# Kernel optimization log

Measured on AMD Instinct MI355X. Metric: run time of the kernel, lower is better.

The kernel has to match this reference:

```python
import jax, jax.numpy as jnp
import numpy as np

B = 8          # batch
RES = 64       # resolution (H = W)
DIM = 512      # channels
HEADS = 8
HD = DIM // HEADS   # 64
HSP, WSP = RES, 8   # idx=0: H_sp=resolution, W_sp=split_size
NH, NW = RES // HSP, RES // WSP   # windows per axis


def setup_inputs() -> dict:
    key = jax.random.key(0)
    k1, k2, k3 = jax.random.split(key, 3)
    qkv = jax.random.normal(k1, (3, B, RES * RES, DIM), dtype=jnp.float32)
    lepe_w = jax.random.normal(k2, (DIM, 1, 3, 3), dtype=jnp.float32) * 0.1
    lepe_b = jax.random.normal(k3, (DIM,), dtype=jnp.float32) * 0.1
    return {"qkv": qkv, "lepe_w": lepe_w, "lepe_b": lepe_b}


def _to_windows(t):
    # [B, L, C] row-major -> [B*NH*NW, HSP*WSP, C]; equivalent to the
    # block-diagonal flex_attention mask grouping (y//H_sp, x//W_sp).
    t = t.reshape(B, NH, HSP, NW, WSP, DIM)
    return t.transpose(0, 1, 3, 2, 4, 5).reshape(B * NH * NW, HSP * WSP, DIM)


def _from_windows(t):
    t = t.reshape(B, NH, NW, HSP, WSP, DIM).transpose(0, 1, 3, 2, 4, 5)
    return t.reshape(B, RES * RES, DIM)


def reference(qkv, lepe_w, lepe_b):
    q, k, v = qkv[0], qkv[1], qkv[2]            # each [B, L, C]
    qw, kw, vw = _to_windows(q), _to_windows(k), _to_windows(v)

    # LePE: depthwise 3x3 conv on v laid out per-window as [n, C, HSP, WSP]
    vimg = vw.transpose(0, 2, 1).reshape(-1, DIM, HSP, WSP)
    lepe = jax.lax.conv_general_dilated(
        vimg, lepe_w, window_strides=(1, 1), padding='SAME',
        dimension_numbers=('NCHW', 'OIHW', 'NCHW'), feature_group_count=DIM)
    lepe = lepe + lepe_b[None, :, None, None]
    lepe = lepe.reshape(-1, DIM, HSP * WSP).transpose(0, 2, 1)  # [n, T, C]

    def split_heads(t):
        return t.reshape(t.shape[0], t.shape[1], HEADS, HD)

    qh, kh, vh, lh = map(split_heads, (qw, kw, vw, lepe))
    scale = 1.0 / np.sqrt(HD).astype(np.float32)  # flex_attention default scale
    scores = jnp.einsum('wqhd,wkhd->whqk', qh, kh) * scale
    attn = jax.nn.softmax(scores, axis=-1)
    out = jnp.einsum('whqk,wkhd->wqhd', attn, vh) + lh   # [n, T, H, hd]
    out = out.reshape(out.shape[0], out.shape[1], DIM)
    return _from_windows(out)
```

## Files before the change

kernel.cpp:

```cpp
#include <hip/hip_runtime.h>
#include <hip/hip_bf16.h>

#define DIMV 512
#define HDV  64
#define VSTR 524
#define VT_BASE 65536
#define SMEM_B (VT_BASE + 64 * VSTR * 2)

typedef __bf16 bf16x8_t __attribute__((ext_vector_type(8)));
typedef float f32x4_t __attribute__((ext_vector_type(4)));

union Frag { bf16x8_t v; unsigned short u[8]; unsigned int w[4]; uint2 d[2]; uint4 q; };

static __device__ __forceinline__ unsigned short f2bf(float f) {
  return __builtin_bit_cast(unsigned short, (__bf16)f);
}
static __device__ __forceinline__ float bf2f(unsigned int h) {
  return __builtin_bit_cast(float, h << 16);
}

#define BARRIER_NODRAIN() asm volatile("s_waitcnt lgkmcnt(0)\n\ts_barrier" ::: "memory")

__global__ __launch_bounds__(1024, 4)
void lepe_attn_kernel(const float* __restrict__ qkv,
                      const float* __restrict__ lw,
                      const float* __restrict__ lb,
                      float* __restrict__ out)
{
  __shared__ __align__(16) unsigned char smem[SMEM_B];

  const int head = blockIdx.x >> 6;
  const int win  = blockIdx.x & 63;
  const int bat  = win >> 3;
  const int nw   = win & 7;

  const int tid  = threadIdx.x;
  const int wave = tid >> 6, lane = tid & 63;
  const int l15  = lane & 15, g = lane >> 4;

  const float* qptr = qkv;
  const float* kptr = qkv + 16777216;
  const float* vptr = qkv + 33554432;
  const int rowbase = bat * 4096;

  auto grow = [&](int tok) -> int {
    return rowbase + ((tok >> 3) << 6) + (nw << 3) + (tok & 7);
  };

  const int s_t = tid >> 4;
  const int s_c = (tid & 15) * 4;
  const size_t GSTRIDE = 262144;
  const float* kg = kptr + (size_t)grow(s_t) * DIMV + head * HDV + s_c;
  const float* vg = vptr + (size_t)grow(s_t) * DIMV + head * HDV + s_c;
  const int kwbase = s_t * 128 + ((s_c * 2) ^ ((s_t & 7) << 4));

  float4 ck0, ck1, cv0, cv1;
  auto issueC = [&](int c) {
    ck0 = *(const float4*)(kg + (size_t)(2 * c) * GSTRIDE);
    ck1 = *(const float4*)(kg + (size_t)(2 * c + 1) * GSTRIDE);
    cv0 = *(const float4*)(vg + (size_t)(2 * c) * GSTRIDE);
    cv1 = *(const float4*)(vg + (size_t)(2 * c + 1) * GSTRIDE);
  };
  auto writeC = [&](int c) {
    uint2 kp;
    kp.x = (unsigned)f2bf(ck0.x) | ((unsigned)f2bf(ck0.y) << 16);
    kp.y = (unsigned)f2bf(ck0.z) | ((unsigned)f2bf(ck0.w) << 16);
    *(uint2*)(smem + (2 * c) * 8192 + kwbase) = kp;
    kp.x = (unsigned)f2bf(ck1.x) | ((unsigned)f2bf(ck1.y) << 16);
    kp.y = (unsigned)f2bf(ck1.z) | ((unsigned)f2bf(ck1.w) << 16);
    *(uint2*)(smem + (2 * c + 1) * 8192 + kwbase) = kp;
    unsigned short* vt = (unsigned short*)(smem + VT_BASE);
    #pragma unroll
    for (int gi = 0; gi < 2; ++gi) {
      const float4 vv = gi ? cv1 : cv0;
      const int t = (2 * c + gi) * 64 + s_t;
      float fv[4] = {vv.x, vv.y, vv.z, vv.w};
      #pragma unroll
      for (int i = 0; i < 4; ++i)
        vt[(s_c + i) * VSTR + t] = f2bf(fv[i]);
    }
  };

  issueC(0);

  const float QSC = 0.1803368801f;
  const int qbase = wave * 32;
  float4 qin[8];
  #pragma unroll
  for (int qi = 0; qi < 2; ++qi) {
    const float* qp = qptr + (size_t)grow(qbase + qi * 16 + l15) * DIMV + head * HDV;
    #pragma unroll
    for (int kc = 0; kc < 2; ++kc) {
      qin[qi * 4 + kc * 2 + 0] = *(const float4*)(qp + kc * 32 + 8 * g);
      qin[qi * 4 + kc * 2 + 1] = *(const float4*)(qp + kc * 32 + 8 * g + 4);
    }
  }

  writeC(0);

  Frag qf[2][2];
  #pragma unroll
  for (int qi = 0; qi < 2; ++qi)
    #pragma unroll
    for (int kc = 0; kc < 2; ++kc) {
      const float4 f0 = qin[qi * 4 + kc * 2 + 0];
      const float4 f1 = qin[qi * 4 + kc * 2 + 1];
      qf[qi][kc].u[0] = f2bf(f0.x * QSC); qf[qi][kc].u[1] = f2bf(f0.y * QSC);
      qf[qi][kc].u[2] = f2bf(f0.z * QSC); qf[qi][kc].u[3] = f2bf(f0.w * QSC);
      qf[qi][kc].u[4] = f2bf(f1.x * QSC); qf[qi][kc].u[5] = f2bf(f1.y * QSC);
      qf[qi][kc].u[6] = f2bf(f1.z * QSC); qf[qi][kc].u[7] = f2bf(f1.w * QSC);
    }

  __syncthreads();

  const f32x4_t zero4 = {0.f, 0.f, 0.f, 0.f};
  f32x4_t ot[4][2];
  #pragma unroll
  for (int di = 0; di < 4; ++di)
    #pragma unroll
    for (int qi = 0; qi < 2; ++qi) ot[di][qi] = zero4;
  float lsumA[2] = {0.f, 0.f};
  float lsumB[2] = {0.f, 0.f};

  const int ksw = (l15 & 7) << 4;

  #pragma unroll
  for (int c = 0; c < 4; ++c) {
    if (c < 3) issueC(c + 1);

    #pragma unroll
    for (int t4 = 0; t4 < 4; ++t4) {
      const int kt = c * 4 + t4;

      Frag kf[2][2];
      #pragma unroll
      for (int ki = 0; ki < 2; ++ki) {
        const unsigned char* rowp = smem + (kt * 32 + ki * 16 + l15) * 128;
        #pragma unroll
        for (int kc = 0; kc < 2; ++kc)
          kf[ki][kc].q = *(const uint4*)(rowp + ((kc * 64 + g * 16) ^ ksw));
      }

      f32x4_t st[2][2];
      #pragma unroll
      for (int ki = 0; ki < 2; ++ki)
        #pragma unroll
        for (int qi = 0; qi < 2; ++qi) st[ki][qi] = zero4;

      #pragma unroll
      for (int kc = 0; kc < 2; ++kc)
        #pragma unroll
        for (int ki = 0; ki < 2; ++ki)
          #pragma unroll
          for (int qi = 0; qi < 2; ++qi)
            st[ki][qi] = __builtin_amdgcn_mfma_f32_16x16x32_bf16(
                kf[ki][kc].v, qf[qi][kc].v, st[ki][qi], 0, 0, 0);

      #pragma unroll
      for (int ki = 0; ki < 2; ++ki)
        #pragma unroll
        for (int qi = 0; qi < 2; ++qi) {
          f32x4_t s = st[ki][qi];
          #pragma unroll
          for (int r = 0; r < 4; ++r) {
            float pr = __builtin_amdgcn_exp2f(s[r]);
            s[r] = pr;
            if (ki == 0) lsumA[qi] += pr;
            else         lsumB[qi] += pr;
          }
          st[ki][qi] = s;
        }

      Frag vf[4];
      #pragma unroll
      for (int di = 0; di < 4; ++di) {
        const unsigned char* vp = smem + VT_BASE + (di * 16 + l15) * (VSTR * 2)
                                  + kt * 64 + 8 * g;
        vf[di].d[0] = *(const uint2*)(vp);
        vf[di].d[1] = *(const uint2*)(vp + 32);
      }

      #pragma unroll
      for (int qi = 0; qi < 2; ++qi) {
        Frag pb;
        #pragma unroll
        for (int r = 0; r < 4; ++r) {
          pb.u[r]     = f2bf(st[0][qi][r]);
          pb.u[4 + r] = f2bf(st[1][qi][r]);
        }
        #pragma unroll
        for (int di = 0; di < 4; ++di)
          ot[di][qi] = __builtin_amdgcn_mfma_f32_16x16x32_bf16(
              vf[di].v, pb.v, ot[di][qi], 0, 0, 0);
      }
    }

    if (c < 3) { writeC(c + 1); BARRIER_NODRAIN(); }
  }

  float rl[2];
  #pragma unroll
  for (int qi = 0; qi < 2; ++qi) {
    float s = lsumA[qi] + lsumB[qi];
    s += __shfl_xor(s, 16, 64);
    s += __shfl_xor(s, 32, 64);
    rl[qi] = 1.0f / s;
  }

  float lout[32];
  {
    float wgt[9];
    const float* wp = lw + (size_t)(head * HDV + lane) * 9;
    #pragma unroll
    for (int i = 0; i < 9; ++i) wgt[i] = wp[i];
    const float bias = lb[head * HDV + lane];
    const int yb = wave * 4;
    const unsigned char* vrow = smem + VT_BASE + lane * (VSTR * 2);

    float rm[8], rc[8], rp2[8];
    auto loadrow = [&](int y, float* dst) {
      if ((unsigned)y < 64u) {
        const unsigned char* pp = vrow + y * 16;
        unsigned a0 = *(const unsigned*)(pp);
        unsigned a1 = *(const unsigned*)(pp + 4);
        unsigned a2 = *(const unsigned*)(pp + 8);
        unsigned a3 = *(const unsigned*)(pp + 12);
        dst[0] = bf2f(a0 & 0xffffu); dst[1] = bf2f(a0 >> 16);
        dst[2] = bf2f(a1 & 0xffffu); dst[3] = bf2f(a1 >> 16);
        dst[4] = bf2f(a2 & 0xffffu); dst[5] = bf2f(a2 >> 16);
        dst[6] = bf2f(a3 & 0xffffu); dst[7] = bf2f(a3 >> 16);
      } else {
        #pragma unroll
        for (int x = 0; x < 8; ++x) dst[x] = 0.f;
      }
    };
    loadrow(yb - 1, rm);
    loadrow(yb, rc);
    #pragma unroll
    for (int yy = 0; yy < 4; ++yy) {
      loadrow(yb + yy + 1, rp2);
      #pragma unroll
      for (int x = 0; x < 8; ++x) {
        float acc = bias;
        if (x > 0) acc += rm[x-1]*wgt[0] + rc[x-1]*wgt[3] + rp2[x-1]*wgt[6];
        acc += rm[x]*wgt[1] + rc[x]*wgt[4] + rp2[x]*wgt[7];
        if (x < 7) acc += rm[x+1]*wgt[2] + rc[x+1]*wgt[5] + rp2[x+1]*wgt[8];
        lout[yy * 8 + x] = acc;
      }
      #pragma unroll
      for (int x = 0; x < 8; ++x) { rm[x] = rc[x]; rc[x] = rp2[x]; }
    }
  }

  BARRIER_NODRAIN();

  unsigned char* bp = smem + wave * 4352;
  #pragma unroll
  for (int t = 0; t < 32; ++t)
    *(unsigned short*)(bp + t * 136 + 2 * lane) = f2bf(lout[t]);
  BARRIER_NODRAIN();

  #pragma unroll
  for (int qi = 0; qi < 2; ++qi) {
    const float rlq = rl[qi];
    const int tl = qi * 16 + l15;
    float* op = out + (size_t)grow(qbase + tl) * DIMV + head * HDV;
    #pragma unroll
    for (int di = 0; di < 4; ++di) {
      uint2 lv = *(const uint2*)(bp + tl * 136 + di * 32 + 8 * g);
      float4 o;
      o.x = ot[di][qi][0] * rlq + bf2f(lv.x & 0xffffu);
      o.y = ot[di][qi][1] * rlq + bf2f(lv.x >> 16);
      o.z = ot[di][qi][2] * rlq + bf2f(lv.y & 0xffffu);
      o.w = ot[di][qi][3] * rlq + bf2f(lv.y >> 16);
      *(float4*)(op + di * 16 + 4 * g) = o;
    }
  }
}

extern "C" void kernel_launch(void* const* d_in, const int* in_sizes, int n_in,
                              void* d_out, int out_size, void* d_ws, size_t ws_size,
                              hipStream_t stream) {
  const float* qkv = (const float*)d_in[0];
  const float* lw  = (const float*)d_in[1];
  const float* lb  = (const float*)d_in[2];
  float* out = (float*)d_out;
  (void)in_sizes; (void)n_in; (void)out_size; (void)d_ws; (void)ws_size;

  dim3 grid(512);
  dim3 block(1024);
  hipLaunchKernelGGL(lepe_attn_kernel, grid, block, 0, stream, qkv, lw, lb, out);
}
```

Baseline: 76.36 us.

## Store K and V in fragment-native swizzled LDS tiles for single 128-bit reads

Reorganizes the shared-memory layout of K and transposed V into per-tile, MFMA-fragment-ordered blocks with XOR swizzles, so each lane reads its K and V operand fragments with one 128-bit LDS load each instead of several smaller strided loads. The store side now computes fragment-ordered addresses, and the LePE convolution row loader is rewritten to read from the new V layout. The aim is fewer LDS instructions and fewer bank conflicts in the inner attention loop. In exchange the scattered 16-bit V stores become more complex, and LDS use changes slightly (128 KB total).

```diff
diff --git a/kernel.cpp b/kernel.cpp
--- a/kernel.cpp
+++ b/kernel.cpp
@@ -3,9 +3,8 @@
 
 #define DIMV 512
 #define HDV  64
-#define VSTR 524
-#define VT_BASE 65536
-#define SMEM_B (VT_BASE + 64 * VSTR * 2)
+#define VBASE 65536
+#define SMEM_B 131072
 
 typedef __bf16 bf16x8_t __attribute__((ext_vector_type(8)));
 typedef float f32x4_t __attribute__((ext_vector_type(4)));
@@ -17,6 +16,12 @@
 }
 static __device__ __forceinline__ float bf2f(unsigned int h) {
   return __builtin_bit_cast(float, h << 16);
+}
+static __device__ __forceinline__ uint2 pack4(const float4 f) {
+  uint2 r;
+  r.x = (unsigned)f2bf(f.x) | ((unsigned)f2bf(f.y) << 16);
+  r.y = (unsigned)f2bf(f.z) | ((unsigned)f2bf(f.w) << 16);
+  return r;
 }
 
 #define BARRIER_NODRAIN() asm volatile("s_waitcnt lgkmcnt(0)\n\ts_barrier" ::: "memory")
@@ -52,7 +57,20 @@
   const size_t GSTRIDE = 262144;
   const float* kg = kptr + (size_t)grow(s_t) * DIMV + head * HDV + s_c;
   const float* vg = vptr + (size_t)grow(s_t) * DIMV + head * HDV + s_c;
-  const int kwbase = s_t * 128 + ((s_c * 2) ^ ((s_t & 7) << 4));
+
+  const int ki_w  = (s_t & 31) >> 4;
+  const int l15k  = s_t & 15;
+  const int kc_w  = s_c >> 5;
+  const int gk_w  = (s_c & 31) >> 3;
+  const int ksw_w = (((kc_w << 1) | (gk_w & 1)) << 5);
+  const int kfoff = ki_w * 2048 + kc_w * 1024
+                  + (((gk_w << 8) | (l15k << 4)) ^ ksw_w) + (s_c & 7) * 2;
+
+  const int di_w = s_c >> 4;
+  const int h_w  = (s_t & 31) >> 4;
+  const int g_w  = (s_t & 15) >> 2;
+  const int r_w  = s_t & 3;
+  const int vtail = h_w * 8 + r_w * 2;
 
   float4 ck0, ck1, cv0, cv1;
   auto issueC = [&](int c) {
@@ -62,22 +80,18 @@
     cv1 = *(const float4*)(vg + (size_t)(2 * c + 1) * GSTRIDE);
   };
   auto writeC = [&](int c) {
-    uint2 kp;
-    kp.x = (unsigned)f2bf(ck0.x) | ((unsigned)f2bf(ck0.y) << 16);
-    kp.y = (unsigned)f2bf(ck0.z) | ((unsigned)f2bf(ck0.w) << 16);
-    *(uint2*)(smem + (2 * c) * 8192 + kwbase) = kp;
-    kp.x = (unsigned)f2bf(ck1.x) | ((unsigned)f2bf(ck1.y) << 16);
-    kp.y = (unsigned)f2bf(ck1.z) | ((unsigned)f2bf(ck1.w) << 16);
-    *(uint2*)(smem + (2 * c + 1) * 8192 + kwbase) = kp;
-    unsigned short* vt = (unsigned short*)(smem + VT_BASE);
     #pragma unroll
     for (int gi = 0; gi < 2; ++gi) {
+      const int tile = 4 * c + 2 * gi + (s_t >> 5);
+      *(uint2*)(smem + tile * 4096 + kfoff) = pack4(gi ? ck1 : ck0);
       const float4 vv = gi ? cv1 : cv0;
-      const int t = (2 * c + gi) * 64 + s_t;
       float fv[4] = {vv.x, vv.y, vv.z, vv.w};
-      #pragma unroll
-      for (int i = 0; i < 4; ++i)
-        vt[(s_c + i) * VSTR + t] = f2bf(fv[i]);
+      unsigned char* vb = smem + VBASE + tile * 4096 + di_w * 1024 + vtail;
+      #pragma unroll
+      for (int i = 0; i < 4; ++i) {
+        const int l15v = (s_c & 15) + i;
+        *(unsigned short*)(vb + ((((g_w << 4) + l15v) ^ di_w) << 4)) = f2bf(fv[i]);
+      }
     }
   };
 
@@ -122,7 +136,10 @@
   float lsumA[2] = {0.f, 0.f};
   float lsumB[2] = {0.f, 0.f};
 
-  const int ksw = (l15 & 7) << 4;
+  const int ksr0 = ((g & 1) << 5);
+  const int ksr1 = ksr0 | 64;
+  const int kread0 = ((lane << 4) ^ ksr0);
+  const int kread1 = 1024 + ((lane << 4) ^ ksr1);
 
   #pragma unroll
   for (int c = 0; c < 4; ++c) {
@@ -131,14 +148,13 @@
     #pragma unroll
     for (int t4 = 0; t4 < 4; ++t4) {
       const int kt = c * 4 + t4;
+      const unsigned char* kb = smem + kt * 4096;
 
       Frag kf[2][2];
       #pragma unroll
       for (int ki = 0; ki < 2; ++ki) {
-        const unsigned char* rowp = smem + (kt * 32 + ki * 16 + l15) * 128;
-        #pragma unroll
-        for (int kc = 0; kc < 2; ++kc)
-          kf[ki][kc].q = *(const uint4*)(rowp + ((kc * 64 + g * 16) ^ ksw));
+        kf[ki][0].q = *(const uint4*)(kb + ki * 2048 + kread0);
+        kf[ki][1].q = *(const uint4*)(kb + ki * 2048 + kread1);
       }
 
       f32x4_t st[2][2];
@@ -173,12 +189,9 @@
 
       Frag vf[4];
       #pragma unroll
-      for (int di = 0; di < 4; ++di) {
-        const unsigned char* vp = smem + VT_BASE + (di * 16 + l15) * (VSTR * 2)
-                                  + kt * 64 + 8 * g;
-        vf[di].d[0] = *(const uint2*)(vp);
-        vf[di].d[1] = *(const uint2*)(vp + 32);
-      }
+      for (int di = 0; di < 4; ++di)
+        vf[di].q = *(const uint4*)(smem + VBASE + kt * 4096 + di * 1024
+                                   + ((lane ^ di) << 4));
 
       #pragma unroll
       for (int qi = 0; qi < 2; ++qi) {
@@ -215,20 +228,22 @@
     for (int i = 0; i < 9; ++i) wgt[i] = wp[i];
     const float bias = lb[head * HDV + lane];
     const int yb = wave * 4;
-    const unsigned char* vrow = smem + VT_BASE + lane * (VSTR * 2);
+    const int dil = lane >> 4;
+    const unsigned char* vrow = smem + VBASE + dil * 1024;
 
     float rm[8], rc[8], rp2[8];
     auto loadrow = [&](int y, float* dst) {
       if ((unsigned)y < 64u) {
-        const unsigned char* pp = vrow + y * 16;
-        unsigned a0 = *(const unsigned*)(pp);
-        unsigned a1 = *(const unsigned*)(pp + 4);
-        unsigned a2 = *(const unsigned*)(pp + 8);
-        unsigned a3 = *(const unsigned*)(pp + 12);
-        dst[0] = bf2f(a0 & 0xffffu); dst[1] = bf2f(a0 >> 16);
-        dst[2] = bf2f(a1 & 0xffffu); dst[3] = bf2f(a1 >> 16);
-        dst[4] = bf2f(a2 & 0xffffu); dst[5] = bf2f(a2 >> 16);
-        dst[6] = bf2f(a3 & 0xffffu); dst[7] = bf2f(a3 >> 16);
+        const int tile = y >> 2;
+        const int hh = (y & 3) >> 1;
+        const int gb = (y & 1) * 2;
+        const unsigned char* pbase = vrow + tile * 4096 + hh * 8;
+        uint2 a = *(const uint2*)(pbase + ((((gb << 4) + l15) ^ dil) << 4));
+        uint2 b = *(const uint2*)(pbase + (((((gb + 1) << 4) + l15) ^ dil) << 4));
+        dst[0] = bf2f(a.x & 0xffffu); dst[1] = bf2f(a.x >> 16);
+        dst[2] = bf2f(a.y & 0xffffu); dst[3] = bf2f(a.y >> 16);
+        dst[4] = bf2f(b.x & 0xffffu); dst[5] = bf2f(b.x >> 16);
+        dst[6] = bf2f(b.y & 0xffffu); dst[7] = bf2f(b.y >> 16);
       } else {
         #pragma unroll
         for (int x = 0; x < 8; ++x) dst[x] = 0.f;
```

New measurement: 75.69 us (median of 2 runs). About the same (-0.9%).
